# Performance work log

Measured on AMD Instinct MI355X. Metric: run time of the kernel, lower is better.

The kernel has to match this reference:

```python
import jax, jax.numpy as jnp
import numpy as np

B, N, F, H, L = 4, 512, 128, 4, 2
HID = 128            # edge MLP hidden width
LAM = 5.0            # sinkhorn_lambda
ITERS = 10           # sinkhorn_iter
NEG_SLOPE = 0.2      # GAT leaky-relu slope


def setup_inputs() -> dict:
    key = jax.random.key(0)
    ks = jax.random.split(key, 10)
    sc = 0.05
    return {
        "joint_features": jax.random.normal(ks[0], (B, N, F), jnp.float32),
        "joint_coords": jax.random.normal(ks[1], (B, N, 3), jnp.float32),
        # edge MLP: Linear(2F+1 -> 128), Linear(128 -> 1)
        "W1": jax.random.normal(ks[2], (2 * F + 1, HID), jnp.float32) * sc,
        "b1": jnp.zeros((HID,), jnp.float32),
        "W2": jax.random.normal(ks[3], (HID, 1), jnp.float32) * sc,
        "b2": jnp.zeros((1,), jnp.float32),
        # GAT layers (stacked over L): W (F -> H*F), attention vecs a_src/a_dst (H,F), bias (F)
        "Wg": jax.random.normal(ks[4], (L, F, H * F), jnp.float32) * sc,
        "a_src": jax.random.normal(ks[5], (L, H, F), jnp.float32) * sc,
        "a_dst": jax.random.normal(ks[6], (L, H, F), jnp.float32) * sc,
        "bg": jnp.zeros((L, F), jnp.float32),
    }


def _forward(joint_features, joint_coords, W1, b1, W2, b2, Wg, a_src, a_dst, bg):
    Bc, Nc, Fc = joint_features.shape
    # pairwise euclidean distances (B,N,N)  == torch.cdist(p=2)
    diff = joint_coords[:, :, None, :] - joint_coords[:, None, :, :]
    dist = jnp.sqrt(jnp.maximum(jnp.sum(diff * diff, axis=-1), 0.0))
    # edge MLP on cat([feat_i, feat_j, dist]). Fuse the concat by splitting W1
    # into row blocks: [W_a (F,HID); W_b (F,HID); w_d (HID,)] -- same math,
    # avoids materializing the (B,N,N,2F+1) concat tensor.
    Wa, Wb, wd = W1[:Fc], W1[Fc:2 * Fc], W1[2 * Fc]
    ha = joint_features @ Wa                      # (B,N,HID)
    hb = joint_features @ Wb                      # (B,N,HID)
    hidden = jax.nn.relu(ha[:, :, None, :] + hb[:, None, :, :]
                         + dist[..., None] * wd + b1)   # (B,N,N,HID)
    cost = jnp.squeeze(hidden @ W2, -1) + b2[0]         # (B,N,N)
    # Sinkhorn normalization: K = exp(-lambda * C), alternate row/col scaling
    def sink_step(P, _):
        P = P / jnp.sum(P, axis=-1, keepdims=True)
        P = P / jnp.sum(P, axis=-2, keepdims=True)
        return P, None
    adj, _ = jax.lax.scan(sink_step, jnp.exp(-LAM * cost), None, length=ITERS)
    # adj is strictly positive -> to_sparse() yields the fully-connected graph
    # per batch; GATConv(heads=H, concat=False) becomes dense attention over N.
    x = joint_features
    nlayers, nheads = Wg.shape[0], a_src.shape[1]
    for l in range(nlayers):
        xw = (x @ Wg[l]).reshape(Bc, Nc, nheads, Fc)            # (B,N,H,F)
        s_src = jnp.einsum('bnhf,hf->bnh', xw, a_src[l])        # sender score
        s_dst = jnp.einsum('bnhf,hf->bnh', xw, a_dst[l])        # receiver score
        # e[b,i,j,h]: message j -> i
        e = jax.nn.leaky_relu(s_dst[:, :, None, :] + s_src[:, None, :, :], NEG_SLOPE)
        attn = jax.nn.softmax(e, axis=2)                        # softmax over senders j
        x = jnp.einsum('bijh,bjhf->bihf', attn, xw).mean(axis=2) + bg[l]
    final_adj = jax.nn.sigmoid(jnp.einsum('bif,bjf->bij', x, x))
    return final_adj, adj


def reference(joint_features, joint_coords, W1, b1, W2, b2, Wg, a_src, a_dst, bg):
    return _forward(joint_features, joint_coords, W1, b1, W2, b2, Wg, a_src, a_dst, bg)
```

## Files before the change

kernel.cpp:

```cpp
#include <hip/hip_runtime.h>
#include <math.h>

#define NB 4
#define NN 512

__global__ void kA(const float* __restrict__ X, const float* __restrict__ W1,
                   const float* __restrict__ b1, float* __restrict__ ha,
                   float* __restrict__ hb, float* __restrict__ ru) {
  int b = blockIdx.y, n0 = blockIdx.x * 8;
  __shared__ float xs[8][128];
  int t = threadIdx.x;
  for (int q = t; q < 1024; q += 128) {
    int r = q >> 7, f = q & 127;
    xs[r][f] = X[(size_t)(b * NN + n0 + r) * 128 + f];
  }
  int flat = b * 64 + blockIdx.x;
  if (flat < 16) ru[flat * 128 + t] = 0.f;
  __syncthreads();
  float accA[8] = {0,0,0,0,0,0,0,0}, accB[8] = {0,0,0,0,0,0,0,0};
  for (int f = 0; f < 128; ++f) {
    float wa = W1[f * 128 + t];
    float wb = W1[(128 + f) * 128 + t];
#pragma unroll
    for (int r = 0; r < 8; ++r) {
      accA[r] = fmaf(xs[r][f], wa, accA[r]);
      accB[r] = fmaf(xs[r][f], wb, accB[r]);
    }
  }
  float b1v = b1[t];
#pragma unroll
  for (int r = 0; r < 8; ++r) {
    ha[(size_t)(b * NN + n0 + r) * 128 + t] = accA[r] + b1v;
    hb[(size_t)(b * NN + n0 + r) * 128 + t] = accB[r];
  }
}

__global__ void kB(const float* __restrict__ ha, const float* __restrict__ hb,
                   const float* __restrict__ coords, const float* __restrict__ W1,
                   const float* __restrict__ W2, const float* __restrict__ b2,
                   float* __restrict__ Km, float* __restrict__ ru) {
  int b = blockIdx.z, i0 = blockIdx.y * 32, j0 = blockIdx.x * 32;
  __shared__ alignas(16) float As[32][132];
  __shared__ alignas(16) float Bs[32][132];
  __shared__ alignas(16) float wd[128];
  __shared__ alignas(16) float w2[128];
  __shared__ float ci[32][3], cj[32][3];
  int t = threadIdx.x;
  for (int q = t; q < 1024; q += 256) {
    int r = q >> 5, c = (q & 31) * 4;
    *(float4*)&As[r][c] = *(const float4*)&ha[(size_t)(b * NN + i0 + r) * 128 + c];
    *(float4*)&Bs[r][c] = *(const float4*)&hb[(size_t)(b * NN + j0 + r) * 128 + c];
  }
  if (t < 128) { wd[t] = W1[256 * 128 + t]; w2[t] = W2[t]; }
  if (t < 96) ((float*)ci)[t] = coords[(size_t)(b * NN + i0) * 3 + t];
  else if (t < 192) ((float*)cj)[t - 96] = coords[(size_t)(b * NN + j0) * 3 + (t - 96)];
  __syncthreads();
  int tx = t & 15, ty = t >> 4;
  int ia = 2 * ty, ib = ia + 1, ja = tx, jb = tx + 16;
  float d00, d01, d10, d11;
  {
    float ax = ci[ia][0], ay = ci[ia][1], az = ci[ia][2];
    float bx = ci[ib][0], by = ci[ib][1], bz = ci[ib][2];
    float cx0 = cj[ja][0], cy0 = cj[ja][1], cz0 = cj[ja][2];
    float cx1 = cj[jb][0], cy1 = cj[jb][1], cz1 = cj[jb][2];
    float dx, dy, dz;
    dx = ax - cx0; dy = ay - cy0; dz = az - cz0;
    d00 = sqrtf(fmaxf(dx * dx + dy * dy + dz * dz, 0.f));
    dx = ax - cx1; dy = ay - cy1; dz = az - cz1;
    d01 = sqrtf(fmaxf(dx * dx + dy * dy + dz * dz, 0.f));
    dx = bx - cx0; dy = by - cy0; dz = bz - cz0;
    d10 = sqrtf(fmaxf(dx * dx + dy * dy + dz * dz, 0.f));
    dx = bx - cx1; dy = by - cy1; dz = bz - cz1;
    d11 = sqrtf(fmaxf(dx * dx + dy * dy + dz * dz, 0.f));
  }
  float a00 = 0, a01 = 0, a10 = 0, a11 = 0;
  for (int k = 0; k < 128; k += 4) {
    float4 A0 = *(float4*)&As[ia][k];
    float4 A1 = *(float4*)&As[ib][k];
    float4 B0 = *(float4*)&Bs[ja][k];
    float4 B1 = *(float4*)&Bs[jb][k];
    float4 W = *(float4*)&wd[k];
    float4 V = *(float4*)&w2[k];
#pragma unroll
    for (int kk = 0; kk < 4; ++kk) {
      float av = ((float*)&A0)[kk], av1 = ((float*)&A1)[kk];
      float bv = ((float*)&B0)[kk], bv1 = ((float*)&B1)[kk];
      float wv = ((float*)&W)[kk], vv = ((float*)&V)[kk];
      float t00 = fmaxf(fmaf(d00, wv, av + bv), 0.f);
      float t01 = fmaxf(fmaf(d01, wv, av + bv1), 0.f);
      float t10 = fmaxf(fmaf(d10, wv, av1 + bv), 0.f);
      float t11 = fmaxf(fmaf(d11, wv, av1 + bv1), 0.f);
      a00 = fmaf(t00, vv, a00);
      a01 = fmaf(t01, vv, a01);
      a10 = fmaf(t10, vv, a10);
      a11 = fmaf(t11, vv, a11);
    }
  }
  float b2v = b2[0];
  float k00 = __expf(-5.0f * (a00 + b2v));
  float k01 = __expf(-5.0f * (a01 + b2v));
  float k10 = __expf(-5.0f * (a10 + b2v));
  float k11 = __expf(-5.0f * (a11 + b2v));
  size_t r0 = (size_t)(b * NN + i0 + ia) * NN + j0;
  size_t r1 = (size_t)(b * NN + i0 + ib) * NN + j0;
  Km[r0 + ja] = k00; Km[r0 + jb] = k01;
  Km[r1 + ja] = k10; Km[r1 + jb] = k11;
  float s0 = k00 + k01, s1 = k10 + k11;
#pragma unroll
  for (int off = 1; off < 16; off <<= 1) {
    s0 += __shfl_xor(s0, off);
    s1 += __shfl_xor(s1, off);
  }
  if (tx == 0) {
    atomicAdd(&ru[b * NN + i0 + ia], s0);
    atomicAdd(&ru[b * NN + i0 + ib], s1);
  }
}


__device__ __forceinline__ void dCcol(const float* __restrict__ Km,
                                      const float* __restrict__ ru,
                                      float* __restrict__ rvp,
                                      float* sm, int ic, int b) {
  float* uinv = sm;
  int t = threadIdx.x;
  if (t < 32) uinv[t] = 1.0f / ru[b * NN + ic * 32 + t];
  __syncthreads();
  const float* Kp = Km + (size_t)(b * NN + ic * 32) * NN + t;
  float acc = 0.f;
#pragma unroll 8
  for (int ii = 0; ii < 32; ++ii) acc = fmaf(Kp[(size_t)ii * NN], uinv[ii], acc);
  rvp[ic * 2048 + b * NN + t] = acc;
}

__device__ __forceinline__ void dCrc(const float* __restrict__ Km,
                                     const float* __restrict__ rvpOld,
                                     float* __restrict__ rvpNew,
                                     float* __restrict__ ru,
                                     float* sm, int ic, int b) {
  float* vinv = sm;
  float* uinv = sm + 512;
  int t = threadIdx.x;
  {
    float s = 0.f;
#pragma unroll
    for (int q = 0; q < 16; ++q) s += rvpOld[q * 2048 + b * NN + t];
    vinv[t] = 1.0f / s;
  }
  __syncthreads();
  int w = t >> 6, l = t & 63;
#pragma unroll
  for (int m = 0; m < 4; ++m) {
    int r = ic * 32 + w * 4 + m;
    const float* Kp = Km + (size_t)(b * NN + r) * NN;
    float acc = 0.f;
#pragma unroll
    for (int mm = 0; mm < 8; ++mm) acc = fmaf(Kp[l + 64 * mm], vinv[l + 64 * mm], acc);
#pragma unroll
    for (int off = 1; off < 64; off <<= 1) acc += __shfl_xor(acc, off);
    if (l == 0) { uinv[w * 4 + m] = 1.0f / acc; ru[b * NN + r] = acc; }
  }
  __syncthreads();
  {
    const float* Kp = Km + (size_t)(b * NN + ic * 32) * NN + t;
    float acc = 0.f;
#pragma unroll 8
    for (int ii = 0; ii < 32; ++ii) acc = fmaf(Kp[(size_t)ii * NN], uinv[ii], acc);
    rvpNew[ic * 2048 + b * NN + t] = acc;
  }
}

__device__ __forceinline__ void dG1f(const float* __restrict__ x,
                                     const float* __restrict__ Wg,
                                     const float* __restrict__ asrc,
                                     const float* __restrict__ adst,
                                     float* __restrict__ xw,
                                     float* __restrict__ ssT,
                                     float* __restrict__ sdT,
                                     float* sm, int bx, int b) {
  int n0 = bx * 8;
  float* xs = sm;
  float* red = sm + 1024;
  int t = threadIdx.x;
  for (int q = t; q < 1024; q += 512)
    xs[q] = x[(size_t)(b * NN + n0 + (q >> 7)) * 128 + (q & 127)];
  __syncthreads();
  int c = t;
  float acc[8] = {0,0,0,0,0,0,0,0};
  for (int f = 0; f < 128; ++f) {
    float w0 = Wg[f * 512 + c];
#pragma unroll
    for (int r = 0; r < 8; ++r) acc[r] = fmaf(xs[r * 128 + f], w0, acc[r]);
  }
#pragma unroll
  for (int r = 0; r < 8; ++r)
    xw[(size_t)(b * NN + n0 + r) * 512 + c] = acc[r];
  float asv = asrc[c], adv = adst[c];
  int w = t >> 6, l = t & 63;
#pragma unroll
  for (int r = 0; r < 8; ++r) {
    float ps = acc[r] * asv, pd = acc[r] * adv;
#pragma unroll
    for (int off = 1; off < 64; off <<= 1) {
      ps += __shfl_xor(ps, off);
      pd += __shfl_xor(pd, off);
    }
    if (l == 0) { red[w * 16 + r * 2] = ps; red[w * 16 + r * 2 + 1] = pd; }
  }
  __syncthreads();
  if (t < 64) {
    int h = t >> 4, rr = t & 7, sd = (t >> 3) & 1;
    float s = red[(2 * h) * 16 + rr * 2 + sd] + red[(2 * h + 1) * 16 + rr * 2 + sd];
    float* dst = sd ? sdT : ssT;
    dst[(size_t)(b * 4 + h) * 512 + n0 + rr] = s;
  }
}

#define PLDV 520
__device__ __forceinline__ void dG2v(const float* __restrict__ xw,
                                     const float* __restrict__ ssT,
                                     const float* __restrict__ sdT,
                                     const float* __restrict__ bg,
                                     float* __restrict__ xo,
                                     float* sm, int bx, int b) {
  int i0 = bx * 8;
  float* pls = sm;
  float* ssb = sm + 8192;
  float* sdl = sm + 8704;
  float* smaxsh = sm + 8736;
  float* mxl = sm + 8744;
  int t = threadIdx.x;
  if (t < 32) {
    int h = t >> 3, r = t & 7;
    sdl[h * 8 + r] = sdT[(size_t)(b * 4 + h) * 512 + i0 + r];
  }
  int fq = t & 31, jh = t >> 5;
  int il = t >> 6, jq = t & 63;
  float4 acc[8];
#pragma unroll
  for (int r = 0; r < 8; ++r) acc[r] = make_float4(0.f, 0.f, 0.f, 0.f);
  for (int h = 0; h < 4; ++h) {
    __syncthreads();
    {
      float v = ssT[(size_t)(b * 4 + h) * 512 + t];
      ssb[t] = v;
#pragma unroll
      for (int off = 1; off < 64; off <<= 1) v = fmaxf(v, __shfl_xor(v, off));
      if ((t & 63) == 0) smaxsh[t >> 6] = v;
    }
    __syncthreads();
    if (t < 8) {
      float m = smaxsh[0];
#pragma unroll
      for (int q = 1; q < 8; ++q) m = fmaxf(m, smaxsh[q]);
      float mm = sdl[h * 8 + t] + m;
      mxl[t] = (mm >= 0.f) ? mm : 0.2f * mm;
    }
    __syncthreads();
    {
      float mx = mxl[il], sdv = sdl[h * 8 + il];
      float pe[8];
      float den = 0.f;
#pragma unroll
      for (int jj = 0; jj < 8; ++jj) {
        int j = jj * 64 + jq;
        float e = sdv + ssb[j];
        e = (e >= 0.f) ? e : 0.2f * e;
        pe[jj] = __expf(e - mx);
        den += pe[jj];
      }
#pragma unroll
      for (int off = 1; off < 64; off <<= 1) den += __shfl_xor(den, off);
      float inv = 1.0f / (4.0f * den);
#pragma unroll
      for (int jj = 0; jj < 8; ++jj) pls[il * PLDV + jj * 64 + jq] = pe[jj] * inv;
    }
    __syncthreads();
    const float* xp = xw + (size_t)(b * NN) * 512 + h * 128 + fq * 4;
    int jbase = jh * 32;
#pragma unroll 4
    for (int jj = 0; jj < 32; ++jj) {
      int j = jbase + jj;
      float4 xv = *(const float4*)&xp[(size_t)j * 512];
#pragma unroll
      for (int r = 0; r < 8; ++r) {
        float p = pls[r * PLDV + j];
        acc[r].x = fmaf(p, xv.x, acc[r].x);
        acc[r].y = fmaf(p, xv.y, acc[r].y);
        acc[r].z = fmaf(p, xv.z, acc[r].z);
        acc[r].w = fmaf(p, xv.w, acc[r].w);
      }
    }
  }
  __syncthreads();
  int w = t >> 6;
#pragma unroll
  for (int r = 0; r < 8; ++r) {
    acc[r].x += __shfl_xor(acc[r].x, 32);
    acc[r].y += __shfl_xor(acc[r].y, 32);
    acc[r].z += __shfl_xor(acc[r].z, 32);
    acc[r].w += __shfl_xor(acc[r].w, 32);
  }
  float4* sc4 = (float4*)pls;
  if ((t & 63) < 32) {
#pragma unroll
    for (int r = 0; r < 8; ++r) sc4[w * 256 + r * 32 + fq] = acc[r];
  }
  __syncthreads();
  if (t < 256) {
    int r = t >> 5, ff = t & 31;
    float4 bb = *(const float4*)&bg[ff * 4];
    float4 s = bb;
#pragma unroll
    for (int q = 0; q < 8; ++q) {
      float4 u = sc4[q * 256 + r * 32 + ff];
      s.x += u.x; s.y += u.y; s.z += u.z; s.w += u.w;
    }
    *(float4*)&xo[(size_t)(b * NN + i0 + r) * 128 + ff * 4] = s;
  }
}

__device__ __forceinline__ void dF(const float* __restrict__ x,
                                   float* __restrict__ out,
                                   float* sm, int fid, int b) {
  int i0 = (fid >> 4) * 32, j0 = (fid & 15) * 32;
  float* As = sm;
  float* Bs = sm + 4224;
  int t = threadIdx.x;
  for (int q = t; q < 1024; q += 512) {
    int r = q >> 5, c = (q & 31) * 4;
    *(float4*)&As[r * 132 + c] = *(const float4*)&x[(size_t)(b * NN + i0 + r) * 128 + c];
    *(float4*)&Bs[r * 132 + c] = *(const float4*)&x[(size_t)(b * NN + j0 + r) * 128 + c];
  }
  __syncthreads();
  int tx = t & 31, ty = t >> 5;
  int ia = 2 * ty, ib = ia + 1;
  float a0 = 0.f, a1 = 0.f;
  for (int k = 0; k < 128; k += 4) {
    float4 A0 = *(float4*)&As[ia * 132 + k];
    float4 A1 = *(float4*)&As[ib * 132 + k];
    float4 B0 = *(float4*)&Bs[tx * 132 + k];
#pragma unroll
    for (int kk = 0; kk < 4; ++kk) {
      a0 = fmaf(((float*)&A0)[kk], ((float*)&B0)[kk], a0);
      a1 = fmaf(((float*)&A1)[kk], ((float*)&B0)[kk], a1);
    }
  }
  out[(size_t)(b * NN + i0 + ia) * NN + j0 + tx] = 1.0f / (1.0f + __expf(-a0));
  out[(size_t)(b * NN + i0 + ib) * NN + j0 + tx] = 1.0f / (1.0f + __expf(-a1));
}


__global__ __launch_bounds__(512) void nCcolG1f(
    const float* Km, const float* ru, float* rvpA,
    const float* X, const float* Wg, const float* as_, const float* ad_,
    float* xw, float* ssT, float* sdT) {
  __shared__ alignas(16) float sm[1280];
  if (blockIdx.x < 16) dCcol(Km, ru, rvpA, sm, blockIdx.x, blockIdx.y);
  else dG1f(X, Wg, as_, ad_, xw, ssT, sdT, sm, blockIdx.x - 16, blockIdx.y);
}

__global__ __launch_bounds__(512) void nCrcG2v(
    const float* Km, const float* rvpOld, float* rvpNew, float* ru,
    const float* xw, const float* ssT, const float* sdT,
    const float* bg, float* xo) {
  __shared__ alignas(16) float sm[8752];
  if (blockIdx.x < 16) dCrc(Km, rvpOld, rvpNew, ru, sm, blockIdx.x, blockIdx.y);
  else dG2v(xw, ssT, sdT, bg, xo, sm, blockIdx.x - 16, blockIdx.y);
}

__global__ __launch_bounds__(512) void nCrcG1f(
    const float* Km, const float* rvpOld, float* rvpNew, float* ru,
    const float* x, const float* Wg, const float* as_, const float* ad_,
    float* xw, float* ssT, float* sdT) {
  __shared__ alignas(16) float sm[1280];
  if (blockIdx.x < 16) dCrc(Km, rvpOld, rvpNew, ru, sm, blockIdx.x, blockIdx.y);
  else dG1f(x, Wg, as_, ad_, xw, ssT, sdT, sm, blockIdx.x - 16, blockIdx.y);
}

__global__ __launch_bounds__(512) void nCrcF(
    const float* Km, const float* rvpOld, float* rvpNew, float* ru,
    const float* x, float* outF) {
  __shared__ alignas(16) float sm[8448];
  if (blockIdx.x < 16) dCrc(Km, rvpOld, rvpNew, ru, sm, blockIdx.x, blockIdx.y);
  else dF(x, outF, sm, blockIdx.x - 16, blockIdx.y);
}

__global__ __launch_bounds__(512) void kCrc(
    const float* Km, const float* rvpOld, float* rvpNew, float* ru) {
  __shared__ alignas(16) float sm[544];
  dCrc(Km, rvpOld, rvpNew, ru, sm, blockIdx.x, blockIdx.y);
}

__global__ __launch_bounds__(512) void kAdj(const float* __restrict__ Km,
                                            const float* __restrict__ ru,
                                            const float* __restrict__ rvp,
                                            float* __restrict__ out) {
  int rc = blockIdx.x, b = blockIdx.y;
  __shared__ float vinv[512];
  __shared__ float uinv[32];
  int t = threadIdx.x;
  {
    float s = 0.f;
#pragma unroll
    for (int ic = 0; ic < 16; ++ic) s += rvp[ic * 2048 + b * NN + t];
    vinv[t] = 1.0f / s;
  }
  if (t < 32) uinv[t] = 1.0f / ru[b * NN + rc * 32 + t];
  __syncthreads();
  float vj = vinv[t];
  const float* Kp = Km + (size_t)(b * NN + rc * 32) * NN + t;
  float* op = out + (size_t)(b * NN + rc * 32) * NN + t;
#pragma unroll 4
  for (int m = 0; m < 32; ++m) {
    op[(size_t)m * NN] = Kp[(size_t)m * NN] * uinv[m] * vj;
  }
}

extern "C" void kernel_launch(void* const* d_in, const int* in_sizes, int n_in,
                              void* d_out, int out_size, void* d_ws, size_t ws_size,
                              hipStream_t stream) {
  (void)in_sizes; (void)n_in; (void)out_size; (void)ws_size;
  const float* X   = (const float*)d_in[0];
  const float* C   = (const float*)d_in[1];
  const float* W1  = (const float*)d_in[2];
  const float* b1  = (const float*)d_in[3];
  const float* W2  = (const float*)d_in[4];
  const float* b2  = (const float*)d_in[5];
  const float* Wg  = (const float*)d_in[6];
  const float* as_ = (const float*)d_in[7];
  const float* ad_ = (const float*)d_in[8];
  const float* bg  = (const float*)d_in[9];
  float* out = (float*)d_out;
  float* ws = (float*)d_ws;

  float* ha    = ws;
  float* hb    = ws + 262144;
  float* Km    = ws + 524288;
  float* ru    = ws + 1572864;
  float* xw    = ws + 1591296;
  float* ssT   = ws + 2639872;
  float* sdT   = ws + 2648064;
  float* x1    = ws + 2656256;
  float* x2    = ws + 2918400;
  float* rvpA  = ws + 3180544;
  float* rvpB  = ws + 3246080;
  float* adj   = out + 1048576;

  kA<<<dim3(64, 4), 128, 0, stream>>>(X, W1, b1, ha, hb, ru);
  kB<<<dim3(16, 16, 4), 256, 0, stream>>>(ha, hb, C, W1, W2, b2, Km, ru);
  nCcolG1f<<<dim3(80, 4), 512, 0, stream>>>(Km, ru, rvpA,
                                            X, Wg, as_, ad_, xw, ssT, sdT);
  nCrcG2v<<<dim3(80, 4), 512, 0, stream>>>(Km, rvpA, rvpB, ru,
                                           xw, ssT, sdT, bg, x1);
  nCrcG1f<<<dim3(80, 4), 512, 0, stream>>>(Km, rvpB, rvpA, ru,
                                           x1, Wg + 65536, as_ + 512, ad_ + 512,
                                           xw, ssT, sdT);
  nCrcG2v<<<dim3(80, 4), 512, 0, stream>>>(Km, rvpA, rvpB, ru,
                                           xw, ssT, sdT, bg + 128, x2);
  nCrcF<<<dim3(272, 4), 512, 0, stream>>>(Km, rvpB, rvpA, ru, x2, out);
  kCrc<<<dim3(16, 4), 512, 0, stream>>>(Km, rvpA, rvpB, ru);
  kCrc<<<dim3(16, 4), 512, 0, stream>>>(Km, rvpB, rvpA, ru);
  kCrc<<<dim3(16, 4), 512, 0, stream>>>(Km, rvpA, rvpB, ru);
  kCrc<<<dim3(16, 4), 512, 0, stream>>>(Km, rvpB, rvpA, ru);
  kCrc<<<dim3(16, 4), 512, 0, stream>>>(Km, rvpA, rvpB, ru);
  kAdj<<<dim3(16, 4), 512, 0, stream>>>(Km, ru, rvpB, adj);
}
```

Measured before the change: 177.8 us.

## Split GAT aggregation per head into separate blocks with a partial-sum reduction kernel

The GAT aggregation kernel previously looped over all 4 heads inside each block, giving only 64 aggregation blocks per batch. It now assigns one head per block (256 blocks per batch), writes per-head partial sums into the output buffer as scratch, and adds a small reduction kernel that sums the heads and adds the bias. The reduction is fused with a Sinkhorn row/col step, so two standalone kCrc launches are removed and the Sinkhorn step count stays the same. The cost is an extra launch per layer and extra global traffic for the partials.

Measured after the change: 165.0 us. -7.2%, faster.

```diff
diff --git a/kernel.cpp b/kernel.cpp
--- a/kernel.cpp
+++ b/kernel.cpp
@@ -216,80 +216,74 @@
   }
 }
 
-#define PLDV 520
-__device__ __forceinline__ void dG2v(const float* __restrict__ xw,
+#define PLT 520
+__device__ __forceinline__ void dG2t(const float* __restrict__ xw,
                                      const float* __restrict__ ssT,
                                      const float* __restrict__ sdT,
-                                     const float* __restrict__ bg,
-                                     float* __restrict__ xo,
+                                     float* __restrict__ partial,
                                      float* sm, int bx, int b) {
-  int i0 = bx * 8;
+  int h = bx & 3, i0 = (bx >> 2) * 8;
+  int bh = b * 4 + h;
   float* pls = sm;
   float* ssb = sm + 8192;
   float* sdl = sm + 8704;
-  float* smaxsh = sm + 8736;
-  float* mxl = sm + 8744;
-  int t = threadIdx.x;
-  if (t < 32) {
-    int h = t >> 3, r = t & 7;
-    sdl[h * 8 + r] = sdT[(size_t)(b * 4 + h) * 512 + i0 + r];
-  }
+  float* smaxsh = sm + 8712;
+  float* mxl = sm + 8720;
+  int t = threadIdx.x;
+  {
+    float v = ssT[(size_t)bh * 512 + t];
+    ssb[t] = v;
+#pragma unroll
+    for (int off = 1; off < 64; off <<= 1) v = fmaxf(v, __shfl_xor(v, off));
+    if ((t & 63) == 0) smaxsh[t >> 6] = v;
+  }
+  if (t < 8) sdl[t] = sdT[(size_t)bh * 512 + i0 + t];
+  __syncthreads();
+  if (t < 8) {
+    float m = smaxsh[0];
+#pragma unroll
+    for (int q = 1; q < 8; ++q) m = fmaxf(m, smaxsh[q]);
+    float mm = sdl[t] + m;
+    mxl[t] = (mm >= 0.f) ? mm : 0.2f * mm;
+  }
+  __syncthreads();
+  {
+    int il = t >> 6, jq = t & 63;
+    float mx = mxl[il], sdv = sdl[il];
+    float pe[8];
+    float den = 0.f;
+#pragma unroll
+    for (int jj = 0; jj < 8; ++jj) {
+      int j = jj * 64 + jq;
+      float e = sdv + ssb[j];
+      e = (e >= 0.f) ? e : 0.2f * e;
+      pe[jj] = __expf(e - mx);
+      den += pe[jj];
+    }
+#pragma unroll
+    for (int off = 1; off < 64; off <<= 1) den += __shfl_xor(den, off);
+    float inv = 1.0f / (4.0f * den);
+#pragma unroll
+    for (int jj = 0; jj < 8; ++jj) pls[il * PLT + jj * 64 + jq] = pe[jj] * inv;
+  }
+  __syncthreads();
   int fq = t & 31, jh = t >> 5;
-  int il = t >> 6, jq = t & 63;
+  const float* xp = xw + (size_t)(b * NN) * 512 + h * 128 + fq * 4;
   float4 acc[8];
 #pragma unroll
   for (int r = 0; r < 8; ++r) acc[r] = make_float4(0.f, 0.f, 0.f, 0.f);
-  for (int h = 0; h < 4; ++h) {
-    __syncthreads();
-    {
-      float v = ssT[(size_t)(b * 4 + h) * 512 + t];
-      ssb[t] = v;
-#pragma unroll
-      for (int off = 1; off < 64; off <<= 1) v = fmaxf(v, __shfl_xor(v, off));
-      if ((t & 63) == 0) smaxsh[t >> 6] = v;
-    }
-    __syncthreads();
-    if (t < 8) {
-      float m = smaxsh[0];
-#pragma unroll
-      for (int q = 1; q < 8; ++q) m = fmaxf(m, smaxsh[q]);
-      float mm = sdl[h * 8 + t] + m;
-      mxl[t] = (mm >= 0.f) ? mm : 0.2f * mm;
-    }
-    __syncthreads();
-    {
-      float mx = mxl[il], sdv = sdl[h * 8 + il];
-      float pe[8];
-      float den = 0.f;
-#pragma unroll
-      for (int jj = 0; jj < 8; ++jj) {
-        int j = jj * 64 + jq;
-        float e = sdv + ssb[j];
-        e = (e >= 0.f) ? e : 0.2f * e;
-        pe[jj] = __expf(e - mx);
-        den += pe[jj];
-      }
-#pragma unroll
-      for (int off = 1; off < 64; off <<= 1) den += __shfl_xor(den, off);
-      float inv = 1.0f / (4.0f * den);
-#pragma unroll
-      for (int jj = 0; jj < 8; ++jj) pls[il * PLDV + jj * 64 + jq] = pe[jj] * inv;
-    }
-    __syncthreads();
-    const float* xp = xw + (size_t)(b * NN) * 512 + h * 128 + fq * 4;
-    int jbase = jh * 32;
+  int jbase = jh * 32;
 #pragma unroll 4
-    for (int jj = 0; jj < 32; ++jj) {
-      int j = jbase + jj;
-      float4 xv = *(const float4*)&xp[(size_t)j * 512];
-#pragma unroll
-      for (int r = 0; r < 8; ++r) {
-        float p = pls[r * PLDV + j];
-        acc[r].x = fmaf(p, xv.x, acc[r].x);
-        acc[r].y = fmaf(p, xv.y, acc[r].y);
-        acc[r].z = fmaf(p, xv.z, acc[r].z);
-        acc[r].w = fmaf(p, xv.w, acc[r].w);
-      }
+  for (int jj = 0; jj < 32; ++jj) {
+    int j = jbase + jj;
+    float4 xv = *(const float4*)&xp[(size_t)j * 512];
+#pragma unroll
+    for (int r = 0; r < 8; ++r) {
+      float p = pls[r * PLT + j];
+      acc[r].x = fmaf(p, xv.x, acc[r].x);
+      acc[r].y = fmaf(p, xv.y, acc[r].y);
+      acc[r].z = fmaf(p, xv.z, acc[r].z);
+      acc[r].w = fmaf(p, xv.w, acc[r].w);
     }
   }
   __syncthreads();
@@ -301,7 +295,7 @@
     acc[r].z += __shfl_xor(acc[r].z, 32);
     acc[r].w += __shfl_xor(acc[r].w, 32);
   }
-  float4* sc4 = (float4*)pls;
+  float4* sc4 = (float4*)sm;
   if ((t & 63) < 32) {
 #pragma unroll
     for (int r = 0; r < 8; ++r) sc4[w * 256 + r * 32 + fq] = acc[r];
@@ -309,15 +303,33 @@
   __syncthreads();
   if (t < 256) {
     int r = t >> 5, ff = t & 31;
-    float4 bb = *(const float4*)&bg[ff * 4];
-    float4 s = bb;
+    float4 s = make_float4(0.f, 0.f, 0.f, 0.f);
 #pragma unroll
     for (int q = 0; q < 8; ++q) {
       float4 u = sc4[q * 256 + r * 32 + ff];
       s.x += u.x; s.y += u.y; s.z += u.z; s.w += u.w;
     }
-    *(float4*)&xo[(size_t)(b * NN + i0 + r) * 128 + ff * 4] = s;
-  }
+    *(float4*)&partial[((size_t)bh * NN + i0 + r) * 128 + ff * 4] = s;
+  }
+}
+
+__device__ __forceinline__ void dRed(const float* __restrict__ partial,
+                                     const float* __restrict__ bg,
+                                     float* __restrict__ xo, int bx, int b) {
+  int idx = bx * 512 + threadIdx.x;
+  int f4 = idx & 31, i = idx >> 5;
+  const float* pp = partial + (((size_t)b * 4) * NN + i) * 128 + f4 * 4;
+  float4 s = *(const float4*)pp;
+  const float* p1 = pp + (size_t)NN * 128;
+  const float* p2 = pp + (size_t)2 * NN * 128;
+  const float* p3 = pp + (size_t)3 * NN * 128;
+  float4 v1 = *(const float4*)p1, v2 = *(const float4*)p2, v3 = *(const float4*)p3;
+  float4 bb = *(const float4*)&bg[f4 * 4];
+  s.x += v1.x + v2.x + v3.x + bb.x;
+  s.y += v1.y + v2.y + v3.y + bb.y;
+  s.z += v1.z + v2.z + v3.z + bb.z;
+  s.w += v1.w + v2.w + v3.w + bb.w;
+  *(float4*)&xo[(size_t)(b * NN + i) * 128 + f4 * 4] = s;
 }
 
 __device__ __forceinline__ void dF(const float* __restrict__ x,
@@ -360,13 +372,20 @@
   else dG1f(X, Wg, as_, ad_, xw, ssT, sdT, sm, blockIdx.x - 16, blockIdx.y);
 }
 
-__global__ __launch_bounds__(512) void nCrcG2v(
+__global__ __launch_bounds__(512) void nCrcG2t(
     const float* Km, const float* rvpOld, float* rvpNew, float* ru,
-    const float* xw, const float* ssT, const float* sdT,
-    const float* bg, float* xo) {
-  __shared__ alignas(16) float sm[8752];
+    const float* xw, const float* ssT, const float* sdT, float* partial) {
+  __shared__ alignas(16) float sm[8728];
   if (blockIdx.x < 16) dCrc(Km, rvpOld, rvpNew, ru, sm, blockIdx.x, blockIdx.y);
-  else dG2v(xw, ssT, sdT, bg, xo, sm, blockIdx.x - 16, blockIdx.y);
+  else dG2t(xw, ssT, sdT, partial, sm, blockIdx.x - 16, blockIdx.y);
+}
+
+__global__ __launch_bounds__(512) void nCrcRed(
+    const float* Km, const float* rvpOld, float* rvpNew, float* ru,
+    const float* partial, const float* bg, float* xo) {
+  __shared__ alignas(16) float sm[544];
+  if (blockIdx.x < 16) dCrc(Km, rvpOld, rvpNew, ru, sm, blockIdx.x, blockIdx.y);
+  else dRed(partial, bg, xo, blockIdx.x - 16, blockIdx.y);
 }
 
 __global__ __launch_bounds__(512) void nCrcG1f(
@@ -446,23 +465,26 @@
   float* rvpA  = ws + 3180544;
   float* rvpB  = ws + 3246080;
   float* adj   = out + 1048576;
+  float* partial = out;
 
   kA<<<dim3(64, 4), 128, 0, stream>>>(X, W1, b1, ha, hb, ru);
   kB<<<dim3(16, 16, 4), 256, 0, stream>>>(ha, hb, C, W1, W2, b2, Km, ru);
   nCcolG1f<<<dim3(80, 4), 512, 0, stream>>>(Km, ru, rvpA,
                                             X, Wg, as_, ad_, xw, ssT, sdT);
-  nCrcG2v<<<dim3(80, 4), 512, 0, stream>>>(Km, rvpA, rvpB, ru,
-                                           xw, ssT, sdT, bg, x1);
-  nCrcG1f<<<dim3(80, 4), 512, 0, stream>>>(Km, rvpB, rvpA, ru,
+  nCrcG2t<<<dim3(272, 4), 512, 0, stream>>>(Km, rvpA, rvpB, ru,
+                                            xw, ssT, sdT, partial);
+  nCrcRed<<<dim3(48, 4), 512, 0, stream>>>(Km, rvpB, rvpA, ru,
+                                           partial, bg, x1);
+  nCrcG1f<<<dim3(80, 4), 512, 0, stream>>>(Km, rvpA, rvpB, ru,
                                            x1, Wg + 65536, as_ + 512, ad_ + 512,
                                            xw, ssT, sdT);
-  nCrcG2v<<<dim3(80, 4), 512, 0, stream>>>(Km, rvpA, rvpB, ru,
-                                           xw, ssT, sdT, bg + 128, x2);
+  nCrcG2t<<<dim3(272, 4), 512, 0, stream>>>(Km, rvpB, rvpA, ru,
+                                            xw, ssT, sdT, partial);
+  nCrcRed<<<dim3(48, 4), 512, 0, stream>>>(Km, rvpA, rvpB, ru,
+                                           partial, bg + 128, x2);
   nCrcF<<<dim3(272, 4), 512, 0, stream>>>(Km, rvpB, rvpA, ru, x2, out);
   kCrc<<<dim3(16, 4), 512, 0, stream>>>(Km, rvpA, rvpB, ru);
   kCrc<<<dim3(16, 4), 512, 0, stream>>>(Km, rvpB, rvpA, ru);
   kCrc<<<dim3(16, 4), 512, 0, stream>>>(Km, rvpA, rvpB, ru);
-  kCrc<<<dim3(16, 4), 512, 0, stream>>>(Km, rvpB, rvpA, ru);
-  kCrc<<<dim3(16, 4), 512, 0, stream>>>(Km, rvpA, rvpB, ru);
   kAdj<<<dim3(16, 4), 512, 0, stream>>>(Km, ru, rvpB, adj);
 }
```
